# Optimization experiments

Measured on AMD Instinct MI355X. Metric: run time of the kernel, lower is better.

## Reference

```python
import jax, jax.numpy as jnp
import numpy as np

B, T, FIN, D = 8, 512, 256, 128


def setup_inputs() -> dict:
    key = jax.random.key(0)
    ks = jax.random.split(key, 12)
    s = lambda fan_in: 1.0 / np.sqrt(fan_in)
    return {
        "x": jax.random.normal(ks[0], (B, T, FIN), jnp.float32),
        "S0": jnp.zeros((B, 1, D, D), jnp.float32),
        "Z0": jnp.zeros((B, 1, D), jnp.float32),
        "gamma": jnp.ones((FIN,), jnp.float32),
        "beta": jnp.zeros((FIN,), jnp.float32),
        "Wk": jax.random.normal(ks[1], (FIN, D), jnp.float32) * s(FIN),
        "Wq": jax.random.normal(ks[2], (FIN, D), jnp.float32) * s(FIN),
        "Wv": jax.random.normal(ks[3], (FIN, D), jnp.float32) * s(FIN),
        "W1": jax.random.normal(ks[4], (D, D), jnp.float32) * s(D),
        "b1": jnp.zeros((D,), jnp.float32),
        "W2": jax.random.normal(ks[5], (D, D), jnp.float32) * s(D),
        "b2": jnp.zeros((D,), jnp.float32),
        "Ws": jax.random.normal(ks[6], (FIN, D), jnp.float32) * s(FIN),
        "bs": jnp.zeros((D,), jnp.float32),
    }


def reference(x, S0, Z0, gamma, beta, Wk, Wq, Wv, W1, b1, W2, b2, Ws, bs):
    CLAMP = 1e20
    # LayerNorm over feature dim
    mu = jnp.mean(x, axis=-1, keepdims=True)
    var = jnp.var(x, axis=-1, keepdims=True)
    xn = (x - mu) / jnp.sqrt(var + 1e-5) * gamma + beta
    # phi(x) = elu(x) + 1
    K = jax.nn.elu(xn @ Wk) + 1.0  # [B,T,D]
    Q = jax.nn.elu(xn @ Wq) + 1.0  # [B,T,D]
    V = xn @ Wv                     # [B,T,D]
    # outer-product state recurrence via cumsum (faithful to original)
    outer = jnp.einsum('bti,btj->btij', K, V)            # [B,T,D,D]
    S = jnp.clip(jnp.cumsum(outer, axis=1), -CLAMP, CLAMP) + S0  # [B,T,D,D]
    Z = jnp.clip(jnp.cumsum(K, axis=1), -CLAMP, CLAMP) + Z0      # [B,T,D]
    numerator = jnp.einsum('bti,btil->btl', Q, S)        # [B,T,D]
    denominator = jnp.einsum('bti,bti->bt', Q, Z)[..., None] + 1e-5
    out = numerator / denominator
    # FFN: relu(relu(out W1 + b1) W2 + b2)
    out = jax.nn.relu(jax.nn.relu(out @ W1 + b1) @ W2 + b2)
    # residual shortcut from normed input
    out = out + xn @ Ws + bs
    S_out = S.reshape(B, T, D * D)
    return out, S_out, Z
```

## Files before the change

kernel.cpp:

```cpp
#include <hip/hip_runtime.h>


constexpr int BB = 8, TT = 512, FIN_ = 256, DD = 128;
constexpr int NROW = BB * TT;
constexpr int CLEN = 64, NCH = 8;
constexpr float CLAMPV = 1e20f;

__global__ __launch_bounds__(256) void ln_kernel(
    const float* __restrict__ x, const float* __restrict__ gamma,
    const float* __restrict__ beta, float* __restrict__ xn)
{
  int tid = threadIdx.x;
  int row = blockIdx.x * 4 + (tid >> 6);
  int lane = tid & 63;
  float4 v = *(const float4*)&x[row * FIN_ + lane * 4];
  float sum = v.x + v.y + v.z + v.w;
  float sq  = v.x * v.x + v.y * v.y + v.z * v.z + v.w * v.w;
#pragma unroll
  for (int off = 1; off < 64; off <<= 1) {
    sum += __shfl_xor(sum, off);
    sq  += __shfl_xor(sq, off);
  }
  float mu  = sum * (1.0f / FIN_);
  float var = sq * (1.0f / FIN_) - mu * mu;
  float rs  = rsqrtf(var + 1e-5f);
  float4 g = *(const float4*)&gamma[lane * 4];
  float4 b = *(const float4*)&beta[lane * 4];
  float4 o;
  o.x = (v.x - mu) * rs * g.x + b.x;
  o.y = (v.y - mu) * rs * g.y + b.y;
  o.z = (v.z - mu) * rs * g.z + b.z;
  o.w = (v.w - mu) * rs * g.w + b.w;
  *(float4*)&xn[row * FIN_ + lane * 4] = o;
}

__global__ __launch_bounds__(256) void gemm_qkvs(
    const float* __restrict__ xn,
    const float* __restrict__ Wk, const float* __restrict__ Wq,
    const float* __restrict__ Wv, const float* __restrict__ Ws,
    const float* __restrict__ bs,
    float* __restrict__ Kb, float* __restrict__ Qb,
    float* __restrict__ Vb, float* __restrict__ Rb)
{
  int ct = blockIdx.x, rt = blockIdx.y;
  int mat = ct >> 1, cb = (ct & 1) * 64;
  const float* W = (mat == 0) ? Wk : (mat == 1) ? Wq : (mat == 2) ? Wv : Ws;
  float* Ob      = (mat == 0) ? Kb : (mat == 1) ? Qb : (mat == 2) ? Vb : Rb;
  __shared__ float As[16][64];
  __shared__ float Bs[16][64];
  int tid = threadIdx.x;
  int tn = tid & 15, tm = tid >> 4;
  int lm = tid >> 2, lq = tid & 3;
  int lk = tid >> 4, ln4 = (tid & 15) * 4;
  float acc[4][4] = {};
  for (int k0 = 0; k0 < FIN_; k0 += 16) {
    float4 av = *(const float4*)&xn[(rt * 64 + lm) * FIN_ + k0 + lq * 4];
    As[lq * 4 + 0][lm] = av.x;
    As[lq * 4 + 1][lm] = av.y;
    As[lq * 4 + 2][lm] = av.z;
    As[lq * 4 + 3][lm] = av.w;
    *(float4*)&Bs[lk][ln4] = *(const float4*)&W[(k0 + lk) * DD + cb + ln4];
    __syncthreads();
#pragma unroll
    for (int k = 0; k < 16; k++) {
      float4 a = *(const float4*)&As[k][tm * 4];
      float4 b = *(const float4*)&Bs[k][tn * 4];
      float ar[4] = {a.x, a.y, a.z, a.w};
      float br[4] = {b.x, b.y, b.z, b.w};
#pragma unroll
      for (int i = 0; i < 4; i++)
#pragma unroll
        for (int j = 0; j < 4; j++) acc[i][j] += ar[i] * br[j];
    }
    __syncthreads();
  }
#pragma unroll
  for (int i = 0; i < 4; i++) {
    int row = rt * 64 + tm * 4 + i;
    int col = cb + tn * 4;
    float vals[4];
#pragma unroll
    for (int j = 0; j < 4; j++) {
      float v = acc[i][j];
      if (mat <= 1) v = (v > 0.f) ? v + 1.f : expf(v);
      else if (mat == 3) v += bs[col + j];
      vals[j] = v;
    }
    float4 o = make_float4(vals[0], vals[1], vals[2], vals[3]);
    *(float4*)&Ob[row * DD + col] = o;
  }
}

__global__ __launch_bounds__(256) void chunksum_kernel(
    const float* __restrict__ Kb, const float* __restrict__ Vb,
    float* __restrict__ chunkS, float* __restrict__ chunkz)
{
  int jt = blockIdx.x, c = blockIdx.y, b = blockIdx.z, tid = threadIdx.x;
  __shared__ float Ks[CLEN][DD];
  __shared__ float Vs[CLEN][32];
  const float* Kc = Kb + (b * TT + c * CLEN) * DD;
  const float* Vc = Vb + (b * TT + c * CLEN) * DD + jt * 32;
  for (int u = 0; u < 8; u++) {
    int idx = u * 256 + tid;
    int t = idx >> 5, c4 = (idx & 31) * 4;
    *(float4*)&Ks[t][c4] = *(const float4*)&Kc[t * DD + c4];
  }
  for (int u = 0; u < 2; u++) {
    int idx = u * 256 + tid;
    int t = idx >> 3, c4 = (idx & 7) * 4;
    *(float4*)&Vs[t][c4] = *(const float4*)&Vc[t * DD + c4];
  }
  __syncthreads();
  int ti = tid >> 3, tj = tid & 7;
  int i0 = ti * 4, jl = tj * 4;
  float acc[4][4] = {};
  for (int t = 0; t < CLEN; t++) {
    float4 kv = *(const float4*)&Ks[t][i0];
    float4 vv = *(const float4*)&Vs[t][jl];
    float kr[4] = {kv.x, kv.y, kv.z, kv.w};
    float vr[4] = {vv.x, vv.y, vv.z, vv.w};
#pragma unroll
    for (int i = 0; i < 4; i++)
#pragma unroll
      for (int j = 0; j < 4; j++) acc[i][j] += kr[i] * vr[j];
  }
  float* oS = chunkS + (b * NCH + c) * DD * DD + jt * 32;
#pragma unroll
  for (int i = 0; i < 4; i++)
    *(float4*)&oS[(i0 + i) * DD + jl] = *(float4*)&acc[i][0];
  if (jt == 0 && tid < DD) {
    float z = 0.f;
    for (int t = 0; t < CLEN; t++) z += Ks[t][tid];
    chunkz[(b * NCH + c) * DD + tid] = z;
  }
}

__global__ __launch_bounds__(256) void scan_s_kernel(
    const float* __restrict__ chunkS, const float* __restrict__ S0,
    float* __restrict__ prefS)
{
  int b = blockIdx.y;
  int idx = blockIdx.x * 256 + threadIdx.x;
  float s0v = S0[b * DD * DD + idx];
  float acc = 0.f;
  for (int c = 0; c < NCH; c++) {
    prefS[(b * NCH + c) * DD * DD + idx] = acc + s0v;
    acc += chunkS[(b * NCH + c) * DD * DD + idx];
  }
}

__global__ __launch_bounds__(128) void scan_z_kernel(
    const float* __restrict__ chunkz, const float* __restrict__ Z0,
    float* __restrict__ prefz)
{
  int b = blockIdx.x, i = threadIdx.x;
  float z0v = Z0[b * DD + i];
  float acc = 0.f;
  for (int c = 0; c < NCH; c++) {
    prefz[(b * NCH + c) * DD + i] = acc + z0v;
    acc += chunkz[(b * NCH + c) * DD + i];
  }
}

__global__ __launch_bounds__(256) void s_write_kernel(
    const float* __restrict__ Kb, const float* __restrict__ Vb,
    const float* __restrict__ prefS, float* __restrict__ Sout)
{
  int it = blockIdx.x, c = blockIdx.y, b = blockIdx.z;
  int i0 = it * 8;
  __shared__ float Vs[CLEN][DD];
  __shared__ float Ksm[CLEN][8];
  int tid = threadIdx.x;
  const float* Kc = Kb + (b * TT + c * CLEN) * DD;
  const float* Vc = Vb + (b * TT + c * CLEN) * DD;
  for (int u = 0; u < 8; u++) {
    int idx = u * 256 + tid;
    int t = idx >> 5, c4 = (idx & 31) * 4;
    *(float4*)&Vs[t][c4] = *(const float4*)&Vc[t * DD + c4];
  }
  for (int u = 0; u < 2; u++) {
    int idx = u * 256 + tid;
    int t = idx >> 3, r = idx & 7;
    Ksm[t][r] = Kc[t * DD + i0 + r];
  }
  __syncthreads();
  int irow = tid >> 5, jq = tid & 31;
  int j = jq * 4;
  float4 pref = *(const float4*)&prefS[(b * NCH + c) * DD * DD + (i0 + irow) * DD + j];
  float4 acc = make_float4(0.f, 0.f, 0.f, 0.f);
  float* So = Sout + (size_t)(b * TT + c * CLEN) * (DD * DD) + (i0 + irow) * DD + j;
  for (int t = 0; t < CLEN; t++) {
    float4 v4 = *(const float4*)&Vs[t][j];
    float kk = Ksm[t][irow];
    acc.x += kk * v4.x; acc.y += kk * v4.y;
    acc.z += kk * v4.z; acc.w += kk * v4.w;
    float4 o;
    o.x = fminf(fmaxf(pref.x + acc.x, -CLAMPV), CLAMPV);
    o.y = fminf(fmaxf(pref.y + acc.y, -CLAMPV), CLAMPV);
    o.z = fminf(fmaxf(pref.z + acc.z, -CLAMPV), CLAMPV);
    o.w = fminf(fmaxf(pref.w + acc.w, -CLAMPV), CLAMPV);
    *(float4*)&So[(size_t)t * (DD * DD)] = o;
  }
}

__global__ __launch_bounds__(256) void attn_kernel(
    const float* __restrict__ Kb, const float* __restrict__ Qb,
    const float* __restrict__ Vb, const float* __restrict__ prefS,
    const float* __restrict__ prefz,
    float* __restrict__ Zout, float* __restrict__ attn_o)
{
  int c = blockIdx.x, b = blockIdx.y, tid = threadIdx.x;
  __shared__ float KsT[DD][CLEN + 1];
  __shared__ float Qs[CLEN][DD + 1];
  __shared__ float sc[CLEN][65];
  __shared__ float zeff[DD];
  __shared__ float den[CLEN];
  const float* Kc = Kb + (b * TT + c * CLEN) * DD;
  const float* Qc = Qb + (b * TT + c * CLEN) * DD;
  const float* Vc = Vb + (b * TT + c * CLEN) * DD;
  for (int u = 0; u < 8; u++) {
    int idx = u * 256 + tid;
    int t = idx >> 5, c4 = (idx & 31) * 4;
    float4 v = *(const float4*)&Kc[t * DD + c4];
    KsT[c4 + 0][t] = v.x; KsT[c4 + 1][t] = v.y;
    KsT[c4 + 2][t] = v.z; KsT[c4 + 3][t] = v.w;
    float4 q = *(const float4*)&Qc[t * DD + c4];
    Qs[t][c4 + 0] = q.x; Qs[t][c4 + 1] = q.y;
    Qs[t][c4 + 2] = q.z; Qs[t][c4 + 3] = q.w;
  }
  if (tid < DD) zeff[tid] = prefz[(b * NCH + c) * DD + tid];
  __syncthreads();
  {
    int tn = tid & 15, tm = tid >> 4;
    float s[4][4] = {};
    for (int k4 = 0; k4 < 32; k4++) {
      float qv[4][4];
#pragma unroll
      for (int i = 0; i < 4; i++)
        *(float4*)&qv[i][0] = *(const float4*)&Qc[(tm * 4 + i) * DD + k4 * 4];
#pragma unroll
      for (int kk = 0; kk < 4; kk++) {
        int k = k4 * 4 + kk;
        float kv[4];
#pragma unroll
        for (int j = 0; j < 4; j++) kv[j] = KsT[k][tn * 4 + j];
#pragma unroll
        for (int i = 0; i < 4; i++)
#pragma unroll
          for (int j = 0; j < 4; j++) s[i][j] += qv[i][kk] * kv[j];
      }
    }
#pragma unroll
    for (int i = 0; i < 4; i++)
#pragma unroll
      for (int j = 0; j < 4; j++) {
        int t = tm * 4 + i, tau = tn * 4 + j;
        sc[t][tau] = (tau <= t) ? s[i][j] : 0.f;
      }
  }
  if (tid < DD) {
    int i = tid;
    float a = zeff[i];
    for (int t = 0; t < CLEN; t++) {
      a += KsT[i][t];
      Zout[(size_t)(b * TT + c * CLEN + t) * DD + i] = fminf(fmaxf(a, -CLAMPV), CLAMPV);
    }
  }
  __syncthreads();
  if (tid < CLEN) {
    int t = tid;
    float d = 0.f;
    for (int tau = 0; tau < CLEN; tau++) d += sc[t][tau];
    float dz = 0.f;
    for (int k = 0; k < DD; k++) dz += Qs[t][k] * zeff[k];
    den[t] = d + dz + 1e-5f;
  }
  __syncthreads();
  int tl = tid & 31, tt = tid >> 5;
  int l0 = tl * 4, t0 = tt * 8;
  float num[8][4] = {};
  for (int tau = 0; tau < CLEN; tau++) {
    float4 v4 = *(const float4*)&Vc[tau * DD + l0];
    float ss[8];
#pragma unroll
    for (int ii = 0; ii < 8; ii++) ss[ii] = sc[t0 + ii][tau];
#pragma unroll
    for (int ii = 0; ii < 8; ii++) {
      num[ii][0] += ss[ii] * v4.x; num[ii][1] += ss[ii] * v4.y;
      num[ii][2] += ss[ii] * v4.z; num[ii][3] += ss[ii] * v4.w;
    }
  }
  const float* P = prefS + (b * NCH + c) * DD * DD;
  for (int i = 0; i < DD; i++) {
    float4 p4 = *(const float4*)&P[i * DD + l0];
    float qq[8];
#pragma unroll
    for (int ii = 0; ii < 8; ii++) qq[ii] = Qs[t0 + ii][i];
#pragma unroll
    for (int ii = 0; ii < 8; ii++) {
      num[ii][0] += qq[ii] * p4.x; num[ii][1] += qq[ii] * p4.y;
      num[ii][2] += qq[ii] * p4.z; num[ii][3] += qq[ii] * p4.w;
    }
  }
  float* og = attn_o + (size_t)(b * TT + c * CLEN) * DD;
#pragma unroll
  for (int ii = 0; ii < 8; ii++) {
    float dd = den[t0 + ii];
    float4 o = make_float4(num[ii][0] / dd, num[ii][1] / dd,
                           num[ii][2] / dd, num[ii][3] / dd);
    *(float4*)&og[(t0 + ii) * DD + l0] = o;
  }
}

__global__ __launch_bounds__(256) void ffn_kernel(
    const float* __restrict__ att, const float* __restrict__ res,
    const float* __restrict__ W1, const float* __restrict__ b1,
    const float* __restrict__ W2, const float* __restrict__ b2,
    float* __restrict__ outp)
{
  int rt = blockIdx.x, tid = threadIdx.x;
  __shared__ float As[32][129];
  __shared__ float H1[32][129];
  const float* ab = att + rt * 32 * DD;
  for (int u = 0; u < 4; u++) {
    int idx = u * 256 + tid;
    int r = idx >> 5, c4 = (idx & 31) * 4;
    float4 v = *(const float4*)&ab[r * DD + c4];
    As[r][c4 + 0] = v.x; As[r][c4 + 1] = v.y;
    As[r][c4 + 2] = v.z; As[r][c4 + 3] = v.w;
  }
  __syncthreads();
  int cn = tid & 31, rm = tid >> 5;
  int col = cn * 4, r0 = rm * 4;
  float acc[4][4] = {};
  for (int k = 0; k < DD; k++) {
    float4 w = *(const float4*)&W1[k * DD + col];
    float a[4];
#pragma unroll
    for (int i = 0; i < 4; i++) a[i] = As[r0 + i][k];
#pragma unroll
    for (int i = 0; i < 4; i++) {
      acc[i][0] += a[i] * w.x; acc[i][1] += a[i] * w.y;
      acc[i][2] += a[i] * w.z; acc[i][3] += a[i] * w.w;
    }
  }
  float4 bv = *(const float4*)&b1[col];
#pragma unroll
  for (int i = 0; i < 4; i++) {
    H1[r0 + i][col + 0] = fmaxf(acc[i][0] + bv.x, 0.f);
    H1[r0 + i][col + 1] = fmaxf(acc[i][1] + bv.y, 0.f);
    H1[r0 + i][col + 2] = fmaxf(acc[i][2] + bv.z, 0.f);
    H1[r0 + i][col + 3] = fmaxf(acc[i][3] + bv.w, 0.f);
  }
  __syncthreads();
  float acc2[4][4] = {};
  for (int k = 0; k < DD; k++) {
    float4 w = *(const float4*)&W2[k * DD + col];
    float a[4];
#pragma unroll
    for (int i = 0; i < 4; i++) a[i] = H1[r0 + i][k];
#pragma unroll
    for (int i = 0; i < 4; i++) {
      acc2[i][0] += a[i] * w.x; acc2[i][1] += a[i] * w.y;
      acc2[i][2] += a[i] * w.z; acc2[i][3] += a[i] * w.w;
    }
  }
  float4 b2v = *(const float4*)&b2[col];
#pragma unroll
  for (int i = 0; i < 4; i++) {
    int row = rt * 32 + r0 + i;
    float4 rv = *(const float4*)&res[row * DD + col];
    float4 o;
    o.x = fmaxf(acc2[i][0] + b2v.x, 0.f) + rv.x;
    o.y = fmaxf(acc2[i][1] + b2v.y, 0.f) + rv.y;
    o.z = fmaxf(acc2[i][2] + b2v.z, 0.f) + rv.z;
    o.w = fmaxf(acc2[i][3] + b2v.w, 0.f) + rv.w;
    *(float4*)&outp[row * DD + col] = o;
  }
}

extern "C" void kernel_launch(void* const* d_in, const int* in_sizes, int n_in,
                              void* d_out, int out_size, void* d_ws, size_t ws_size,
                              hipStream_t stream)
{
  const float* x     = (const float*)d_in[0];
  const float* S0    = (const float*)d_in[1];
  const float* Z0    = (const float*)d_in[2];
  const float* gamma = (const float*)d_in[3];
  const float* beta  = (const float*)d_in[4];
  const float* Wk    = (const float*)d_in[5];
  const float* Wq    = (const float*)d_in[6];
  const float* Wv    = (const float*)d_in[7];
  const float* W1    = (const float*)d_in[8];
  const float* b1    = (const float*)d_in[9];
  const float* W2    = (const float*)d_in[10];
  const float* b2    = (const float*)d_in[11];
  const float* Ws    = (const float*)d_in[12];
  const float* bs    = (const float*)d_in[13];

  float* out_main = (float*)d_out;
  float* Sout = out_main + NROW * DD;
  float* Zout = Sout + (size_t)NROW * DD * DD;

  float* ws_f   = (float*)d_ws;
  float* xn     = ws_f;
  float* Kb     = xn + 1048576;
  float* Qb     = Kb + 524288;
  float* Vb     = Qb + 524288;
  float* Rb     = Vb + 524288;
  float* chunkS = Rb + 524288;
  float* prefS  = chunkS + 1048576;
  float* chunkz = prefS + 1048576;
  float* prefz  = chunkz + 8192;
  float* attn_o = prefz + 8192;

  ln_kernel<<<NROW / 4, 256, 0, stream>>>(x, gamma, beta, xn);
  gemm_qkvs<<<dim3(8, 64), 256, 0, stream>>>(xn, Wk, Wq, Wv, Ws, bs, Kb, Qb, Vb, Rb);
  chunksum_kernel<<<dim3(4, NCH, BB), 256, 0, stream>>>(Kb, Vb, chunkS, chunkz);
  scan_s_kernel<<<dim3(64, BB), 256, 0, stream>>>(chunkS, S0, prefS);
  scan_z_kernel<<<BB, 128, 0, stream>>>(chunkz, Z0, prefz);
  s_write_kernel<<<dim3(16, NCH, BB), 256, 0, stream>>>(Kb, Vb, prefS, Sout);
  attn_kernel<<<dim3(NCH, BB), 256, 0, stream>>>(Kb, Qb, Vb, prefS, prefz, Zout, attn_o);
  ffn_kernel<<<NROW / 32, 256, 0, stream>>>(attn_o, Rb, W1, b1, W2, b2, out_main);
}
```

Measured before the change: 420.0 us.

## Split attention per sub-chunk, fuse scan kernels, nontemporal S stores, smaller FFN tiles

Splits the attention kernel so each block handles 16 query rows of a chunk, raising the grid from 64 to 256 blocks and using a causal bound on the score loop. The two scan kernels are merged into one launch, the S output and Z output use nontemporal stores, and the FFN kernel uses 16-row tiles with 128 threads to get more blocks. The aim is better GPU occupancy on a low-parallelism attention stage, one fewer launch, and less cache pollution from the large S write. In exchange each attention block reloads K and prefS, which adds redundant global traffic.

```diff
diff --git a/kernel.cpp b/kernel.cpp
--- a/kernel.cpp
+++ b/kernel.cpp
@@ -5,6 +5,8 @@
 constexpr int NROW = BB * TT;
 constexpr int CLEN = 64, NCH = 8;
 constexpr float CLAMPV = 1e20f;
+
+typedef float f4v __attribute__((ext_vector_type(4)));
 
 __global__ __launch_bounds__(256) void ln_kernel(
     const float* __restrict__ x, const float* __restrict__ gamma,
@@ -135,30 +137,31 @@
   }
 }
 
-__global__ __launch_bounds__(256) void scan_s_kernel(
+__global__ __launch_bounds__(256) void scan_kernel(
     const float* __restrict__ chunkS, const float* __restrict__ S0,
-    float* __restrict__ prefS)
+    float* __restrict__ prefS,
+    const float* __restrict__ chunkz, const float* __restrict__ Z0,
+    float* __restrict__ prefz)
 {
   int b = blockIdx.y;
+  if (blockIdx.x == 64) {
+    int i = threadIdx.x;
+    if (i < DD) {
+      float z0v = Z0[b * DD + i];
+      float acc = 0.f;
+      for (int c = 0; c < NCH; c++) {
+        prefz[(b * NCH + c) * DD + i] = acc + z0v;
+        acc += chunkz[(b * NCH + c) * DD + i];
+      }
+    }
+    return;
+  }
   int idx = blockIdx.x * 256 + threadIdx.x;
   float s0v = S0[b * DD * DD + idx];
   float acc = 0.f;
   for (int c = 0; c < NCH; c++) {
     prefS[(b * NCH + c) * DD * DD + idx] = acc + s0v;
     acc += chunkS[(b * NCH + c) * DD * DD + idx];
-  }
-}
-
-__global__ __launch_bounds__(128) void scan_z_kernel(
-    const float* __restrict__ chunkz, const float* __restrict__ Z0,
-    float* __restrict__ prefz)
-{
-  int b = blockIdx.x, i = threadIdx.x;
-  float z0v = Z0[b * DD + i];
-  float acc = 0.f;
-  for (int c = 0; c < NCH; c++) {
-    prefz[(b * NCH + c) * DD + i] = acc + z0v;
-    acc += chunkz[(b * NCH + c) * DD + i];
   }
 }
 
@@ -189,17 +192,18 @@
   float4 pref = *(const float4*)&prefS[(b * NCH + c) * DD * DD + (i0 + irow) * DD + j];
   float4 acc = make_float4(0.f, 0.f, 0.f, 0.f);
   float* So = Sout + (size_t)(b * TT + c * CLEN) * (DD * DD) + (i0 + irow) * DD + j;
+#pragma unroll 4
   for (int t = 0; t < CLEN; t++) {
     float4 v4 = *(const float4*)&Vs[t][j];
     float kk = Ksm[t][irow];
     acc.x += kk * v4.x; acc.y += kk * v4.y;
     acc.z += kk * v4.z; acc.w += kk * v4.w;
-    float4 o;
-    o.x = fminf(fmaxf(pref.x + acc.x, -CLAMPV), CLAMPV);
-    o.y = fminf(fmaxf(pref.y + acc.y, -CLAMPV), CLAMPV);
-    o.z = fminf(fmaxf(pref.z + acc.z, -CLAMPV), CLAMPV);
-    o.w = fminf(fmaxf(pref.w + acc.w, -CLAMPV), CLAMPV);
-    *(float4*)&So[(size_t)t * (DD * DD)] = o;
+    f4v o4;
+    o4.x = fminf(fmaxf(pref.x + acc.x, -CLAMPV), CLAMPV);
+    o4.y = fminf(fmaxf(pref.y + acc.y, -CLAMPV), CLAMPV);
+    o4.z = fminf(fmaxf(pref.z + acc.z, -CLAMPV), CLAMPV);
+    o4.w = fminf(fmaxf(pref.w + acc.w, -CLAMPV), CLAMPV);
+    __builtin_nontemporal_store(o4, (f4v*)&So[(size_t)t * (DD * DD)]);
   }
 }
 
@@ -209,121 +213,108 @@
     const float* __restrict__ prefz,
     float* __restrict__ Zout, float* __restrict__ attn_o)
 {
-  int c = blockIdx.x, b = blockIdx.y, tid = threadIdx.x;
+  int sub = blockIdx.x, c = blockIdx.y, b = blockIdx.z, tid = threadIdx.x;
+  int t0 = sub * 16;
+  int tlim = t0 + 16;
   __shared__ float KsT[DD][CLEN + 1];
-  __shared__ float Qs[CLEN][DD + 1];
-  __shared__ float sc[CLEN][65];
+  __shared__ float Qs[16][DD + 1];
+  __shared__ float sc[16][CLEN + 1];
   __shared__ float zeff[DD];
-  __shared__ float den[CLEN];
+  __shared__ float den[16];
   const float* Kc = Kb + (b * TT + c * CLEN) * DD;
   const float* Qc = Qb + (b * TT + c * CLEN) * DD;
   const float* Vc = Vb + (b * TT + c * CLEN) * DD;
-  for (int u = 0; u < 8; u++) {
-    int idx = u * 256 + tid;
+  for (int idx = tid; idx < tlim * 32; idx += 256) {
     int t = idx >> 5, c4 = (idx & 31) * 4;
     float4 v = *(const float4*)&Kc[t * DD + c4];
     KsT[c4 + 0][t] = v.x; KsT[c4 + 1][t] = v.y;
     KsT[c4 + 2][t] = v.z; KsT[c4 + 3][t] = v.w;
-    float4 q = *(const float4*)&Qc[t * DD + c4];
-    Qs[t][c4 + 0] = q.x; Qs[t][c4 + 1] = q.y;
-    Qs[t][c4 + 2] = q.z; Qs[t][c4 + 3] = q.w;
+  }
+  for (int idx = tid; idx < 16 * 32; idx += 256) {
+    int r = idx >> 5, c4 = (idx & 31) * 4;
+    float4 q = *(const float4*)&Qc[(t0 + r) * DD + c4];
+    Qs[r][c4 + 0] = q.x; Qs[r][c4 + 1] = q.y;
+    Qs[r][c4 + 2] = q.z; Qs[r][c4 + 3] = q.w;
   }
   if (tid < DD) zeff[tid] = prefz[(b * NCH + c) * DD + tid];
   __syncthreads();
   {
-    int tn = tid & 15, tm = tid >> 4;
-    float s[4][4] = {};
-    for (int k4 = 0; k4 < 32; k4++) {
-      float qv[4][4];
-#pragma unroll
-      for (int i = 0; i < 4; i++)
-        *(float4*)&qv[i][0] = *(const float4*)&Qc[(tm * 4 + i) * DD + k4 * 4];
-#pragma unroll
-      for (int kk = 0; kk < 4; kk++) {
-        int k = k4 * 4 + kk;
-        float kv[4];
-#pragma unroll
-        for (int j = 0; j < 4; j++) kv[j] = KsT[k][tn * 4 + j];
-#pragma unroll
-        for (int i = 0; i < 4; i++)
-#pragma unroll
-          for (int j = 0; j < 4; j++) s[i][j] += qv[i][kk] * kv[j];
+    int tm = tid >> 4, tn = tid & 15;
+    if (tn * 4 < tlim) {
+      float s0 = 0.f, s1 = 0.f, s2 = 0.f, s3 = 0.f;
+#pragma unroll 4
+      for (int k = 0; k < DD; k++) {
+        float q = Qs[tm][k];
+        s0 += q * KsT[k][tn * 4 + 0];
+        s1 += q * KsT[k][tn * 4 + 1];
+        s2 += q * KsT[k][tn * 4 + 2];
+        s3 += q * KsT[k][tn * 4 + 3];
       }
-    }
-#pragma unroll
-    for (int i = 0; i < 4; i++)
-#pragma unroll
-      for (int j = 0; j < 4; j++) {
-        int t = tm * 4 + i, tau = tn * 4 + j;
-        sc[t][tau] = (tau <= t) ? s[i][j] : 0.f;
-      }
-  }
-  if (tid < DD) {
+      int t = t0 + tm;
+      sc[tm][tn * 4 + 0] = (tn * 4 + 0 <= t) ? s0 : 0.f;
+      sc[tm][tn * 4 + 1] = (tn * 4 + 1 <= t) ? s1 : 0.f;
+      sc[tm][tn * 4 + 2] = (tn * 4 + 2 <= t) ? s2 : 0.f;
+      sc[tm][tn * 4 + 3] = (tn * 4 + 3 <= t) ? s3 : 0.f;
+    }
+  }
+  __syncthreads();
+  if (tid < 16) {
+    int t = t0 + tid;
+    float d = 0.f;
+    for (int tau = 0; tau <= t; tau++) d += sc[tid][tau];
+    float dz = 0.f;
+    for (int k = 0; k < DD; k++) dz += Qs[tid][k] * zeff[k];
+    den[tid] = d + dz + 1e-5f;
+  }
+  __syncthreads();
+  int tl = tid & 31, tg = tid >> 5;
+  int l0 = tl * 4, r0 = tg * 2, r1 = tg * 2 + 1;
+  float n0[4] = {}, n1[4] = {};
+  for (int tau = 0; tau < tlim; tau++) {
+    float4 v4 = *(const float4*)&Vc[tau * DD + l0];
+    float sa = sc[r0][tau], sb = sc[r1][tau];
+    n0[0] += sa * v4.x; n0[1] += sa * v4.y; n0[2] += sa * v4.z; n0[3] += sa * v4.w;
+    n1[0] += sb * v4.x; n1[1] += sb * v4.y; n1[2] += sb * v4.z; n1[3] += sb * v4.w;
+  }
+  const float* P = prefS + (b * NCH + c) * DD * DD;
+#pragma unroll 2
+  for (int i = 0; i < DD; i++) {
+    float4 p4 = *(const float4*)&P[i * DD + l0];
+    float qa = Qs[r0][i], qb = Qs[r1][i];
+    n0[0] += qa * p4.x; n0[1] += qa * p4.y; n0[2] += qa * p4.z; n0[3] += qa * p4.w;
+    n1[0] += qb * p4.x; n1[1] += qb * p4.y; n1[2] += qb * p4.z; n1[3] += qb * p4.w;
+  }
+  float* og = attn_o + (size_t)(b * TT + c * CLEN + t0) * DD;
+  {
+    float da = den[r0], db = den[r1];
+    float4 oa = make_float4(n0[0] / da, n0[1] / da, n0[2] / da, n0[3] / da);
+    float4 ob = make_float4(n1[0] / db, n1[1] / db, n1[2] / db, n1[3] / db);
+    *(float4*)&og[r0 * DD + l0] = oa;
+    *(float4*)&og[r1 * DD + l0] = ob;
+  }
+  if (sub == 3 && tid < DD) {
     int i = tid;
     float a = zeff[i];
     for (int t = 0; t < CLEN; t++) {
       a += KsT[i][t];
-      Zout[(size_t)(b * TT + c * CLEN + t) * DD + i] = fminf(fmaxf(a, -CLAMPV), CLAMPV);
-    }
-  }
-  __syncthreads();
-  if (tid < CLEN) {
-    int t = tid;
-    float d = 0.f;
-    for (int tau = 0; tau < CLEN; tau++) d += sc[t][tau];
-    float dz = 0.f;
-    for (int k = 0; k < DD; k++) dz += Qs[t][k] * zeff[k];
-    den[t] = d + dz + 1e-5f;
-  }
-  __syncthreads();
-  int tl = tid & 31, tt = tid >> 5;
-  int l0 = tl * 4, t0 = tt * 8;
-  float num[8][4] = {};
-  for (int tau = 0; tau < CLEN; tau++) {
-    float4 v4 = *(const float4*)&Vc[tau * DD + l0];
-    float ss[8];
-#pragma unroll
-    for (int ii = 0; ii < 8; ii++) ss[ii] = sc[t0 + ii][tau];
-#pragma unroll
-    for (int ii = 0; ii < 8; ii++) {
-      num[ii][0] += ss[ii] * v4.x; num[ii][1] += ss[ii] * v4.y;
-      num[ii][2] += ss[ii] * v4.z; num[ii][3] += ss[ii] * v4.w;
-    }
-  }
-  const float* P = prefS + (b * NCH + c) * DD * DD;
-  for (int i = 0; i < DD; i++) {
-    float4 p4 = *(const float4*)&P[i * DD + l0];
-    float qq[8];
-#pragma unroll
-    for (int ii = 0; ii < 8; ii++) qq[ii] = Qs[t0 + ii][i];
-#pragma unroll
-    for (int ii = 0; ii < 8; ii++) {
-      num[ii][0] += qq[ii] * p4.x; num[ii][1] += qq[ii] * p4.y;
-      num[ii][2] += qq[ii] * p4.z; num[ii][3] += qq[ii] * p4.w;
-    }
-  }
-  float* og = attn_o + (size_t)(b * TT + c * CLEN) * DD;
-#pragma unroll
-  for (int ii = 0; ii < 8; ii++) {
-    float dd = den[t0 + ii];
-    float4 o = make_float4(num[ii][0] / dd, num[ii][1] / dd,
-                           num[ii][2] / dd, num[ii][3] / dd);
-    *(float4*)&og[(t0 + ii) * DD + l0] = o;
-  }
-}
-
-__global__ __launch_bounds__(256) void ffn_kernel(
+      a = fminf(fmaxf(a, -CLAMPV), CLAMPV);
+      __builtin_nontemporal_store(a, &Zout[(size_t)(b * TT + c * CLEN + t) * DD + i]);
+    }
+  }
+}
+
+__global__ __launch_bounds__(128) void ffn_kernel(
     const float* __restrict__ att, const float* __restrict__ res,
     const float* __restrict__ W1, const float* __restrict__ b1,
     const float* __restrict__ W2, const float* __restrict__ b2,
     float* __restrict__ outp)
 {
   int rt = blockIdx.x, tid = threadIdx.x;
-  __shared__ float As[32][129];
-  __shared__ float H1[32][129];
-  const float* ab = att + rt * 32 * DD;
+  __shared__ float As[16][129];
+  __shared__ float H1[16][129];
+  const float* ab = att + rt * 16 * DD;
   for (int u = 0; u < 4; u++) {
-    int idx = u * 256 + tid;
+    int idx = u * 128 + tid;
     int r = idx >> 5, c4 = (idx & 31) * 4;
     float4 v = *(const float4*)&ab[r * DD + c4];
     As[r][c4 + 0] = v.x; As[r][c4 + 1] = v.y;
@@ -368,7 +359,7 @@
   float4 b2v = *(const float4*)&b2[col];
 #pragma unroll
   for (int i = 0; i < 4; i++) {
-    int row = rt * 32 + r0 + i;
+    int row = rt * 16 + r0 + i;
     float4 rv = *(const float4*)&res[row * DD + col];
     float4 o;
     o.x = fmaxf(acc2[i][0] + b2v.x, 0.f) + rv.x;
@@ -417,9 +408,8 @@
   ln_kernel<<<NROW / 4, 256, 0, stream>>>(x, gamma, beta, xn);
   gemm_qkvs<<<dim3(8, 64), 256, 0, stream>>>(xn, Wk, Wq, Wv, Ws, bs, Kb, Qb, Vb, Rb);
   chunksum_kernel<<<dim3(4, NCH, BB), 256, 0, stream>>>(Kb, Vb, chunkS, chunkz);
-  scan_s_kernel<<<dim3(64, BB), 256, 0, stream>>>(chunkS, S0, prefS);
-  scan_z_kernel<<<BB, 128, 0, stream>>>(chunkz, Z0, prefz);
+  scan_kernel<<<dim3(65, BB), 256, 0, stream>>>(chunkS, S0, prefS, chunkz, Z0, prefz);
   s_write_kernel<<<dim3(16, NCH, BB), 256, 0, stream>>>(Kb, Vb, prefS, Sout);
-  attn_kernel<<<dim3(NCH, BB), 256, 0, stream>>>(Kb, Qb, Vb, prefS, prefz, Zout, attn_o);
-  ffn_kernel<<<NROW / 32, 256, 0, stream>>>(attn_o, Rb, W1, b1, W2, b2, out_main);
-}
+  attn_kernel<<<dim3(4, NCH, BB), 256, 0, stream>>>(Kb, Qb, Vb, prefS, prefz, Zout, attn_o);
+  ffn_kernel<<<NROW / 16, 128, 0, stream>>>(attn_o, Rb, W1, b1, W2, b2, out_main);
+}
```

New measurement: 413.6 us. No clear change (-1.5%).
